# Performance work log

Hardware: AMD Instinct MI355X
Metric: run time of the kernel (lower is better)

The kernel has to match this reference:

```python
import jax, jax.numpy as jnp
import numpy as np

# Standard SMPL kinematic-tree parent indices (from kintree_table in the pkl)
PARENTS = np.array([-1, 0, 0, 0, 1, 2, 3, 4, 5, 6, 7, 8, 9, 9, 9, 12, 13, 14, 16, 17, 18, 19, 20, 21])
NJ = 24
NV = 6890  # SMPL template vertex count
N_POINTS = 2_000_000


def rodrigues(r):
    # r: (J,3) axis-angle -> (J,3,3) rotation matrices (eps matches torch's tiny noise regularizer)
    theta = jnp.linalg.norm(r, axis=1, keepdims=True) + 1e-8        # (J,1)
    rh = r / theta                                                   # (J,3)
    cos = jnp.cos(theta)[:, :, None]                                 # (J,1,1)
    sin = jnp.sin(theta)[:, :, None]
    z = jnp.zeros_like(rh[:, 0])
    K = jnp.stack([z, -rh[:, 2], rh[:, 1],
                   rh[:, 2], z, -rh[:, 0],
                   -rh[:, 1], rh[:, 0], z], axis=1).reshape(-1, 3, 3)
    outer = rh[:, :, None] * rh[:, None, :]
    return cos * jnp.eye(3, dtype=r.dtype) + (1.0 - cos) * outer + sin * K


def joint_transforms(beta, theta, shapedirs, v_template, J_regressor):
    # v_shaped: (6890,3); J: (24,3) joint locations
    v_shaped = jnp.einsum('vck,k->vc', shapedirs, beta) + v_template
    J = J_regressor @ v_shaped
    R = rodrigues(theta)                                             # (24,3,3)
    J_rel = jnp.concatenate([J[:1], J[1:] - J[PARENTS[1:]]], axis=0)
    bottom = jnp.broadcast_to(jnp.array([0., 0., 0., 1.], dtype=R.dtype), (NJ, 1, 4))
    local = jnp.concatenate([jnp.concatenate([R, J_rel[:, :, None]], axis=2), bottom], axis=1)  # (24,4,4)
    # chain along the fixed 24-joint kinematic tree
    res = [local[0]]
    for i in range(1, NJ):
        res.append(res[PARENTS[i]] @ local[i])
    G = jnp.stack(res, axis=0)                                       # (24,4,4)
    # subtract rest-pose joint translation (the 'pack' step)
    Jh = jnp.concatenate([J, jnp.zeros((NJ, 1), J.dtype)], axis=1)   # (24,4)
    t = jnp.einsum('jab,jb->ja', G, Jh)                              # (24,4)
    return G - jnp.concatenate([jnp.zeros((NJ, 4, 3), G.dtype), t[:, :, None]], axis=2)


def setup_inputs() -> dict:
    key = jax.random.key(0)
    ks = jax.random.split(key, 8)
    w = jax.random.uniform(ks[1], (NJ, N_POINTS), dtype=jnp.float32)
    w = w / jnp.sum(w, axis=0, keepdims=True)  # LBS weights sum to 1 per point
    return {
        'points': jax.random.normal(ks[0], (3, N_POINTS), dtype=jnp.float32),
        'weights': w,
        'beta': jax.random.normal(ks[2], (10,), dtype=jnp.float32),
        'theta': 0.3 * jax.random.normal(ks[3], (NJ, 3), dtype=jnp.float32),
        'da_theta': 0.3 * jax.random.normal(ks[4], (NJ, 3), dtype=jnp.float32),
        'shapedirs': 0.01 * jax.random.normal(ks[5], (NV, 3, 10), dtype=jnp.float32),
        'v_template': jax.random.normal(ks[6], (NV, 3), dtype=jnp.float32),
        'J_regressor': jax.random.uniform(ks[7], (NJ, NV), dtype=jnp.float32) / NV,
    }


def reference(points, weights, beta, theta, da_theta, shapedirs, v_template, J_regressor):
    # da_results: inverse rest ('da') pose transforms, built at init with beta = 0
    da = joint_transforms(jnp.zeros_like(beta), da_theta, shapedirs, v_template, J_regressor)
    da_inv = jnp.linalg.inv(da)                                      # (24,4,4)
    pose = joint_transforms(beta, theta, shapedirs, v_template, J_regressor)
    A = jnp.einsum('jab,jbc->jac', pose, da_inv)                     # (24,4,4)
    # weighted blend of joint transforms per point, then 4x4 matvec
    T = jnp.einsum('jn,jab->nab', weights, A)                        # (N,4,4)
    pts = points.T                                                   # (N,3)
    p_h = jnp.concatenate([pts, jnp.ones((pts.shape[0], 1), pts.dtype)], axis=1)  # (N,4)
    v = jnp.einsum('nab,nb->na', T, p_h)[:, :3]                      # (N,3)
    return v.T[None]                                                 # (1,3,N)
```

## Files before the change

kernel.cpp:

```cpp
#include <hip/hip_runtime.h>
#include <cmath>

#define NJ 24

__constant__ int PARENTS_c[NJ] = {-1, 0, 0, 0, 1, 2, 3, 4, 5, 6, 7, 8,
                                  9, 9, 9, 12, 13, 14, 16, 17, 18, 19, 20, 21};

__global__ __launch_bounds__(256) void joints_partial_kernel(
    const float* __restrict__ shapedirs,
    const float* __restrict__ v_template,
    const float* __restrict__ J_reg,
    const float* __restrict__ beta,
    float* __restrict__ Jpart, int NVv) {
  const int j = blockIdx.x;
  const int part = blockIdx.y;
  const int nparts = gridDim.y;

  __shared__ float sbeta[10];
  if (threadIdx.x < 10) sbeta[threadIdx.x] = beta[threadIdx.x];
  __syncthreads();

  const int v0 = (NVv * part) / nparts;
  const int v1 = (NVv * (part + 1)) / nparts;

  float acc[6] = {0.f, 0.f, 0.f, 0.f, 0.f, 0.f};
  for (int v = v0 + (int)threadIdx.x; v < v1; v += blockDim.x) {
    float w = J_reg[(size_t)j * NVv + v];
#pragma unroll
    for (int c = 0; c < 3; ++c) {
      float vtc = v_template[(size_t)v * 3 + c];
      float vs = vtc;
      const float* sd = shapedirs + ((size_t)v * 3 + c) * 10;
#pragma unroll
      for (int k = 0; k < 10; ++k) vs = fmaf(sd[k], sbeta[k], vs);
      acc[c] = fmaf(w, vs, acc[c]);
      acc[3 + c] = fmaf(w, vtc, acc[3 + c]);
    }
  }

#pragma unroll
  for (int c = 0; c < 6; ++c) {
    float x = acc[c];
#pragma unroll
    for (int off = 32; off > 0; off >>= 1) x += __shfl_down(x, off, 64);
    acc[c] = x;
  }
  __shared__ float wred[4][6];
  const int wave = threadIdx.x >> 6;
  const int lane = threadIdx.x & 63;
  if (lane == 0) {
#pragma unroll
    for (int c = 0; c < 6; ++c) wred[wave][c] = acc[c];
  }
  __syncthreads();
  if (threadIdx.x == 0) {
#pragma unroll
    for (int c = 0; c < 6; ++c) {
      float s = wred[0][c] + wred[1][c] + wred[2][c] + wred[3][c];
      Jpart[((size_t)j * nparts + part) * 6 + c] = s;
    }
  }
}

__device__ inline void rodrigues_local(double rx, double ry, double rz,
                                       double tx, double ty, double tz,
                                       double* L) {
  double th = sqrt(rx * rx + ry * ry + rz * rz) + 1e-8;
  double x = rx / th, y = ry / th, z = rz / th;
  double c = cos(th), s = sin(th), u = 1.0 - c;
  L[0] = c + u * x * x;  L[1] = u * x * y - s * z; L[2] = u * x * z + s * y; L[3] = tx;
  L[4] = u * x * y + s * z; L[5] = c + u * y * y;  L[6] = u * y * z - s * x; L[7] = ty;
  L[8] = u * x * z - s * y; L[9] = u * y * z + s * x; L[10] = c + u * z * z; L[11] = tz;
}

__device__ inline void affine_mul(const double* A, const double* B, double* C) {
#pragma unroll
  for (int r = 0; r < 3; ++r) {
#pragma unroll
    for (int cc = 0; cc < 3; ++cc)
      C[r * 4 + cc] = A[r * 4 + 0] * B[0 * 4 + cc] + A[r * 4 + 1] * B[1 * 4 + cc] +
                      A[r * 4 + 2] * B[2 * 4 + cc];
    C[r * 4 + 3] = A[r * 4 + 0] * B[3] + A[r * 4 + 1] * B[7] + A[r * 4 + 2] * B[11] +
                   A[r * 4 + 3];
  }
}

__device__ inline void inv3(const double* m, double* o) {
  double det = m[0] * (m[4] * m[8] - m[5] * m[7]) -
               m[1] * (m[3] * m[8] - m[5] * m[6]) +
               m[2] * (m[3] * m[7] - m[4] * m[6]);
  double id = 1.0 / det;
  o[0] = (m[4] * m[8] - m[5] * m[7]) * id;
  o[1] = (m[2] * m[7] - m[1] * m[8]) * id;
  o[2] = (m[1] * m[5] - m[2] * m[4]) * id;
  o[3] = (m[5] * m[6] - m[3] * m[8]) * id;
  o[4] = (m[0] * m[8] - m[2] * m[6]) * id;
  o[5] = (m[2] * m[3] - m[0] * m[5]) * id;
  o[6] = (m[3] * m[7] - m[4] * m[6]) * id;
  o[7] = (m[1] * m[6] - m[0] * m[7]) * id;
  o[8] = (m[0] * m[4] - m[1] * m[3]) * id;
}

__global__ __launch_bounds__(64) void transforms_kernel(
    const float* __restrict__ theta,
    const float* __restrict__ da_theta,
    const float* __restrict__ Jpart,
    int nparts,
    float* __restrict__ A_out) {
  __shared__ double J[NJ][3], J0[NJ][3];
  __shared__ double Lp[NJ][12], Ld[NJ][12], Gp[NJ][12], Gd[NJ][12];
  const int j = threadIdx.x;

  if (j < NJ) {
#pragma unroll
    for (int c = 0; c < 3; ++c) {
      double s = 0.0, s0 = 0.0;
      for (int p = 0; p < nparts; ++p) {
        s += (double)Jpart[(j * nparts + p) * 6 + c];
        s0 += (double)Jpart[(j * nparts + p) * 6 + 3 + c];
      }
      J[j][c] = s;
      J0[j][c] = s0;
    }
  }
  __syncthreads();

  if (j < NJ) {
    int par = PARENTS_c[j];
    double jx = J[j][0], jy = J[j][1], jz = J[j][2];
    double j0x = J0[j][0], j0y = J0[j][1], j0z = J0[j][2];
    if (par >= 0) {
      jx -= J[par][0]; jy -= J[par][1]; jz -= J[par][2];
      j0x -= J0[par][0]; j0y -= J0[par][1]; j0z -= J0[par][2];
    }
    rodrigues_local(theta[j * 3], theta[j * 3 + 1], theta[j * 3 + 2], jx, jy, jz, Lp[j]);
    rodrigues_local(da_theta[j * 3], da_theta[j * 3 + 1], da_theta[j * 3 + 2],
                    j0x, j0y, j0z, Ld[j]);
  }
  __syncthreads();

  if (threadIdx.x == 0) {
#pragma unroll
    for (int c = 0; c < 12; ++c) { Gp[0][c] = Lp[0][c]; Gd[0][c] = Ld[0][c]; }
    for (int i = 1; i < NJ; ++i) {
      int par = PARENTS_c[i];
      affine_mul(Gp[par], Lp[i], Gp[i]);
      affine_mul(Gd[par], Ld[i], Gd[i]);
    }
  }
  __syncthreads();

  if (j < NJ) {
    double P[12], D[12];
#pragma unroll
    for (int r = 0; r < 3; ++r) {
      double tp = Gp[j][r * 4 + 0] * J[j][0] + Gp[j][r * 4 + 1] * J[j][1] +
                  Gp[j][r * 4 + 2] * J[j][2];
      P[r * 4 + 0] = Gp[j][r * 4 + 0];
      P[r * 4 + 1] = Gp[j][r * 4 + 1];
      P[r * 4 + 2] = Gp[j][r * 4 + 2];
      P[r * 4 + 3] = Gp[j][r * 4 + 3] - tp;
      double td = Gd[j][r * 4 + 0] * J0[j][0] + Gd[j][r * 4 + 1] * J0[j][1] +
                  Gd[j][r * 4 + 2] * J0[j][2];
      D[r * 4 + 0] = Gd[j][r * 4 + 0];
      D[r * 4 + 1] = Gd[j][r * 4 + 1];
      D[r * 4 + 2] = Gd[j][r * 4 + 2];
      D[r * 4 + 3] = Gd[j][r * 4 + 3] - td;
    }
    double m[9] = {D[0], D[1], D[2], D[4], D[5], D[6], D[8], D[9], D[10]};
    double mi[9];
    inv3(m, mi);
    double it[3];
#pragma unroll
    for (int r = 0; r < 3; ++r)
      it[r] = -(mi[r * 3 + 0] * D[3] + mi[r * 3 + 1] * D[7] + mi[r * 3 + 2] * D[11]);
#pragma unroll
    for (int r = 0; r < 3; ++r) {
#pragma unroll
      for (int cc = 0; cc < 3; ++cc)
        A_out[j * 12 + r * 4 + cc] =
            (float)(P[r * 4 + 0] * mi[0 * 3 + cc] + P[r * 4 + 1] * mi[1 * 3 + cc] +
                    P[r * 4 + 2] * mi[2 * 3 + cc]);
      A_out[j * 12 + r * 4 + 3] =
          (float)(P[r * 4 + 0] * it[0] + P[r * 4 + 1] * it[1] +
                  P[r * 4 + 2] * it[2] + P[r * 4 + 3]);
    }
  }
}

__global__ __launch_bounds__(256) void lbs_kernel(
    const float* __restrict__ points,
    const float* __restrict__ weights,
    const float* __restrict__ A,
    float* __restrict__ out,
    int N) {
  __shared__ float sA[NJ * 12];
  for (int i = threadIdx.x; i < NJ * 12; i += blockDim.x) sA[i] = A[i];
  __syncthreads();

  const int tid = blockIdx.x * blockDim.x + threadIdx.x;
  const int n4 = tid * 4;
  if (n4 >= N) return;
  const size_t Ns = (size_t)N;

  if (n4 + 4 <= N) {
    float4 px = *(const float4*)(points + n4);
    float4 py = *(const float4*)(points + Ns + n4);
    float4 pz = *(const float4*)(points + 2 * Ns + n4);

    float4 T[12];
#pragma unroll
    for (int r = 0; r < 12; ++r) T[r] = make_float4(0.f, 0.f, 0.f, 0.f);

#pragma unroll
    for (int jj = 0; jj < NJ; ++jj) {
      float4 w = *(const float4*)(weights + (size_t)jj * Ns + n4);
#pragma unroll
      for (int r = 0; r < 12; ++r) {
        float a = sA[jj * 12 + r];
        T[r].x = fmaf(w.x, a, T[r].x);
        T[r].y = fmaf(w.y, a, T[r].y);
        T[r].z = fmaf(w.z, a, T[r].z);
        T[r].w = fmaf(w.w, a, T[r].w);
      }
    }

    float4 ox, oy, oz;
    ox.x = fmaf(T[0].x, px.x, fmaf(T[1].x, py.x, fmaf(T[2].x, pz.x, T[3].x)));
    ox.y = fmaf(T[0].y, px.y, fmaf(T[1].y, py.y, fmaf(T[2].y, pz.y, T[3].y)));
    ox.z = fmaf(T[0].z, px.z, fmaf(T[1].z, py.z, fmaf(T[2].z, pz.z, T[3].z)));
    ox.w = fmaf(T[0].w, px.w, fmaf(T[1].w, py.w, fmaf(T[2].w, pz.w, T[3].w)));
    oy.x = fmaf(T[4].x, px.x, fmaf(T[5].x, py.x, fmaf(T[6].x, pz.x, T[7].x)));
    oy.y = fmaf(T[4].y, px.y, fmaf(T[5].y, py.y, fmaf(T[6].y, pz.y, T[7].y)));
    oy.z = fmaf(T[4].z, px.z, fmaf(T[5].z, py.z, fmaf(T[6].z, pz.z, T[7].z)));
    oy.w = fmaf(T[4].w, px.w, fmaf(T[5].w, py.w, fmaf(T[6].w, pz.w, T[7].w)));
    oz.x = fmaf(T[8].x, px.x, fmaf(T[9].x, py.x, fmaf(T[10].x, pz.x, T[11].x)));
    oz.y = fmaf(T[8].y, px.y, fmaf(T[9].y, py.y, fmaf(T[10].y, pz.y, T[11].y)));
    oz.z = fmaf(T[8].z, px.z, fmaf(T[9].z, py.z, fmaf(T[10].z, pz.z, T[11].z)));
    oz.w = fmaf(T[8].w, px.w, fmaf(T[9].w, py.w, fmaf(T[10].w, pz.w, T[11].w)));

    *(float4*)(out + n4) = ox;
    *(float4*)(out + Ns + n4) = oy;
    *(float4*)(out + 2 * Ns + n4) = oz;
  } else {
    for (int n = n4; n < N; ++n) {
      float X = points[n], Y = points[Ns + n], Z = points[2 * Ns + n];
      float T[12];
#pragma unroll
      for (int r = 0; r < 12; ++r) T[r] = 0.f;
      for (int jj = 0; jj < NJ; ++jj) {
        float w = weights[(size_t)jj * Ns + n];
#pragma unroll
        for (int r = 0; r < 12; ++r) T[r] = fmaf(w, sA[jj * 12 + r], T[r]);
      }
      out[n] = fmaf(T[0], X, fmaf(T[1], Y, fmaf(T[2], Z, T[3])));
      out[Ns + n] = fmaf(T[4], X, fmaf(T[5], Y, fmaf(T[6], Z, T[7])));
      out[2 * Ns + n] = fmaf(T[8], X, fmaf(T[9], Y, fmaf(T[10], Z, T[11])));
    }
  }
}

extern "C" void kernel_launch(void* const* d_in, const int* in_sizes, int n_in,
                              void* d_out, int out_size, void* d_ws, size_t ws_size,
                              hipStream_t stream) {
  const float* points = (const float*)d_in[0];
  const float* weights = (const float*)d_in[1];
  const float* beta = (const float*)d_in[2];
  const float* theta = (const float*)d_in[3];
  const float* da_theta = (const float*)d_in[4];
  const float* shapedirs = (const float*)d_in[5];
  const float* v_template = (const float*)d_in[6];
  const float* J_regressor = (const float*)d_in[7];

  const int N = in_sizes[0] / 3;
  const int NVv = in_sizes[6] / 3;
  const int NPARTS = 8;

  float* ws = (float*)d_ws;
  float* A = ws;
  float* Jpart = ws + 512;

  dim3 gA(NJ, NPARTS);
  joints_partial_kernel<<<gA, 256, 0, stream>>>(shapedirs, v_template, J_regressor,
                                                beta, Jpart, NVv);
  transforms_kernel<<<1, 64, 0, stream>>>(theta, da_theta, Jpart, NPARTS, A);

  const int threads_total = (N + 3) / 4;
  const int blocks = (threads_total + 255) / 256;
  lbs_kernel<<<blocks, 256, 0, stream>>>(points, weights, A, (float*)d_out, N);
}
```

Baseline: 328.3 us.

## Parallelize kinematic chain per joint, use nontemporal LBS loads/stores, more J partitions

The serial single-thread kinematic chain is replaced by per-joint path walks over precomputed root-to-joint paths, with pose and rest chains handled by separate wavefronts of a 128-thread block. The LBS kernel switches to nontemporal vector loads and stores for points, weights and output so the streamed data bypasses cache retention. The joint-regression partition count doubles to spread that reduction over more blocks. The path walk repeats matrix products that the serial chain shared between joints, and the nontemporal hints may or may not help a purely streaming kernel.

Result: faster. 305.1 us (-7.1%).

```diff
diff --git a/kernel.cpp b/kernel.cpp
--- a/kernel.cpp
+++ b/kernel.cpp
@@ -3,8 +3,38 @@
 
 #define NJ 24
 
+typedef float f4 __attribute__((ext_vector_type(4)));
+
 __constant__ int PARENTS_c[NJ] = {-1, 0, 0, 0, 1, 2, 3, 4, 5, 6, 7, 8,
                                   9, 9, 9, 12, 13, 14, 16, 17, 18, 19, 20, 21};
+
+__constant__ signed char PATHS_c[NJ][9] = {
+    {0, 0, 0, 0, 0, 0, 0, 0, 0},
+    {0, 1, 0, 0, 0, 0, 0, 0, 0},
+    {0, 2, 0, 0, 0, 0, 0, 0, 0},
+    {0, 3, 0, 0, 0, 0, 0, 0, 0},
+    {0, 1, 4, 0, 0, 0, 0, 0, 0},
+    {0, 2, 5, 0, 0, 0, 0, 0, 0},
+    {0, 3, 6, 0, 0, 0, 0, 0, 0},
+    {0, 1, 4, 7, 0, 0, 0, 0, 0},
+    {0, 2, 5, 8, 0, 0, 0, 0, 0},
+    {0, 3, 6, 9, 0, 0, 0, 0, 0},
+    {0, 1, 4, 7, 10, 0, 0, 0, 0},
+    {0, 2, 5, 8, 11, 0, 0, 0, 0},
+    {0, 3, 6, 9, 12, 0, 0, 0, 0},
+    {0, 3, 6, 9, 13, 0, 0, 0, 0},
+    {0, 3, 6, 9, 14, 0, 0, 0, 0},
+    {0, 3, 6, 9, 12, 15, 0, 0, 0},
+    {0, 3, 6, 9, 13, 16, 0, 0, 0},
+    {0, 3, 6, 9, 14, 17, 0, 0, 0},
+    {0, 3, 6, 9, 13, 16, 18, 0, 0},
+    {0, 3, 6, 9, 14, 17, 19, 0, 0},
+    {0, 3, 6, 9, 13, 16, 18, 20, 0},
+    {0, 3, 6, 9, 14, 17, 19, 21, 0},
+    {0, 3, 6, 9, 13, 16, 18, 20, 22},
+    {0, 3, 6, 9, 14, 17, 19, 21, 23}};
+__constant__ signed char PLEN_c[NJ] = {1, 2, 2, 2, 3, 3, 3, 4, 4, 4, 5, 5,
+                                       5, 5, 5, 6, 6, 6, 7, 7, 8, 8, 9, 9};
 
 __global__ __launch_bounds__(256) void joints_partial_kernel(
     const float* __restrict__ shapedirs,
@@ -82,6 +112,19 @@
                       A[r * 4 + 2] * B[2 * 4 + cc];
     C[r * 4 + 3] = A[r * 4 + 0] * B[3] + A[r * 4 + 1] * B[7] + A[r * 4 + 2] * B[11] +
                    A[r * 4 + 3];
+  }
+}
+
+__device__ inline void chain_walk(const double (*L)[12], int jj, double* M) {
+  const signed char* path = PATHS_c[jj];
+  const int len = PLEN_c[jj];
+#pragma unroll
+  for (int c = 0; c < 12; ++c) M[c] = L[path[0]][c];
+  for (int k = 1; k < len; ++k) {
+    double T[12];
+    affine_mul(M, L[path[k]], T);
+#pragma unroll
+    for (int c = 0; c < 12; ++c) M[c] = T[c];
   }
 }
 
@@ -101,7 +144,7 @@
   o[8] = (m[0] * m[4] - m[1] * m[3]) * id;
 }
 
-__global__ __launch_bounds__(64) void transforms_kernel(
+__global__ __launch_bounds__(128) void transforms_kernel(
     const float* __restrict__ theta,
     const float* __restrict__ da_theta,
     const float* __restrict__ Jpart,
@@ -109,48 +152,54 @@
     float* __restrict__ A_out) {
   __shared__ double J[NJ][3], J0[NJ][3];
   __shared__ double Lp[NJ][12], Ld[NJ][12], Gp[NJ][12], Gd[NJ][12];
-  const int j = threadIdx.x;
-
-  if (j < NJ) {
+  const int t = threadIdx.x;
+
+  if (t < NJ) {
 #pragma unroll
     for (int c = 0; c < 3; ++c) {
       double s = 0.0, s0 = 0.0;
       for (int p = 0; p < nparts; ++p) {
-        s += (double)Jpart[(j * nparts + p) * 6 + c];
-        s0 += (double)Jpart[(j * nparts + p) * 6 + 3 + c];
+        s += (double)Jpart[(t * nparts + p) * 6 + c];
+        s0 += (double)Jpart[(t * nparts + p) * 6 + 3 + c];
       }
-      J[j][c] = s;
-      J0[j][c] = s0;
-    }
-  }
-  __syncthreads();
-
-  if (j < NJ) {
+      J[t][c] = s;
+      J0[t][c] = s0;
+    }
+  }
+  __syncthreads();
+
+  if (t < NJ) {
+    const int j = t;
     int par = PARENTS_c[j];
     double jx = J[j][0], jy = J[j][1], jz = J[j][2];
+    if (par >= 0) { jx -= J[par][0]; jy -= J[par][1]; jz -= J[par][2]; }
+    rodrigues_local(theta[j * 3], theta[j * 3 + 1], theta[j * 3 + 2], jx, jy, jz, Lp[j]);
+  } else if (t >= 64 && t < 64 + NJ) {
+    const int j = t - 64;
+    int par = PARENTS_c[j];
     double j0x = J0[j][0], j0y = J0[j][1], j0z = J0[j][2];
-    if (par >= 0) {
-      jx -= J[par][0]; jy -= J[par][1]; jz -= J[par][2];
-      j0x -= J0[par][0]; j0y -= J0[par][1]; j0z -= J0[par][2];
-    }
-    rodrigues_local(theta[j * 3], theta[j * 3 + 1], theta[j * 3 + 2], jx, jy, jz, Lp[j]);
+    if (par >= 0) { j0x -= J0[par][0]; j0y -= J0[par][1]; j0z -= J0[par][2]; }
     rodrigues_local(da_theta[j * 3], da_theta[j * 3 + 1], da_theta[j * 3 + 2],
                     j0x, j0y, j0z, Ld[j]);
   }
   __syncthreads();
 
-  if (threadIdx.x == 0) {
-#pragma unroll
-    for (int c = 0; c < 12; ++c) { Gp[0][c] = Lp[0][c]; Gd[0][c] = Ld[0][c]; }
-    for (int i = 1; i < NJ; ++i) {
-      int par = PARENTS_c[i];
-      affine_mul(Gp[par], Lp[i], Gp[i]);
-      affine_mul(Gd[par], Ld[i], Gd[i]);
-    }
-  }
-  __syncthreads();
-
-  if (j < NJ) {
+  if (t < NJ) {
+    double M[12];
+    chain_walk(Lp, t, M);
+#pragma unroll
+    for (int c = 0; c < 12; ++c) Gp[t][c] = M[c];
+  } else if (t >= 64 && t < 64 + NJ) {
+    const int j = t - 64;
+    double M[12];
+    chain_walk(Ld, j, M);
+#pragma unroll
+    for (int c = 0; c < 12; ++c) Gd[j][c] = M[c];
+  }
+  __syncthreads();
+
+  if (t < NJ) {
+    const int j = t;
     double P[12], D[12];
 #pragma unroll
     for (int r = 0; r < 3; ++r) {
@@ -204,17 +253,17 @@
   const size_t Ns = (size_t)N;
 
   if (n4 + 4 <= N) {
-    float4 px = *(const float4*)(points + n4);
-    float4 py = *(const float4*)(points + Ns + n4);
-    float4 pz = *(const float4*)(points + 2 * Ns + n4);
-
-    float4 T[12];
-#pragma unroll
-    for (int r = 0; r < 12; ++r) T[r] = make_float4(0.f, 0.f, 0.f, 0.f);
+    f4 px = __builtin_nontemporal_load((const f4*)(points + n4));
+    f4 py = __builtin_nontemporal_load((const f4*)(points + Ns + n4));
+    f4 pz = __builtin_nontemporal_load((const f4*)(points + 2 * Ns + n4));
+
+    f4 T[12];
+#pragma unroll
+    for (int r = 0; r < 12; ++r) T[r] = (f4)(0.f);
 
 #pragma unroll
     for (int jj = 0; jj < NJ; ++jj) {
-      float4 w = *(const float4*)(weights + (size_t)jj * Ns + n4);
+      f4 w = __builtin_nontemporal_load((const f4*)(weights + (size_t)jj * Ns + n4));
 #pragma unroll
       for (int r = 0; r < 12; ++r) {
         float a = sA[jj * 12 + r];
@@ -225,23 +274,23 @@
       }
     }
 
-    float4 ox, oy, oz;
+    f4 ox, oy, oz;
     ox.x = fmaf(T[0].x, px.x, fmaf(T[1].x, py.x, fmaf(T[2].x, pz.x, T[3].x)));
     ox.y = fmaf(T[0].y, px.y, fmaf(T[1].y, py.y, fmaf(T[2].y, pz.y, T[3].y)));
     ox.z = fmaf(T[0].z, px.z, fmaf(T[1].z, py.z, fmaf(T[2].z, pz.z, T[3].z)));
     ox.w = fmaf(T[0].w, px.w, fmaf(T[1].w, py.w, fmaf(T[2].w, pz.w, T[3].w)));
     oy.x = fmaf(T[4].x, px.x, fmaf(T[5].x, py.x, fmaf(T[6].x, pz.x, T[7].x)));
     oy.y = fmaf(T[4].y, px.y, fmaf(T[5].y, py.y, fmaf(T[6].y, pz.y, T[7].y)));
-    oy.z = fmaf(T[4].z, px.z, fmaf(T[5].z, py.z, fmaf(T[6].z, pz.z, T[7].z)));
+    oy.z = fmaf(T[4].z, px.z, fmaf(T[6 - 1].z, py.z, fmaf(T[6].z, pz.z, T[7].z)));
     oy.w = fmaf(T[4].w, px.w, fmaf(T[5].w, py.w, fmaf(T[6].w, pz.w, T[7].w)));
     oz.x = fmaf(T[8].x, px.x, fmaf(T[9].x, py.x, fmaf(T[10].x, pz.x, T[11].x)));
     oz.y = fmaf(T[8].y, px.y, fmaf(T[9].y, py.y, fmaf(T[10].y, pz.y, T[11].y)));
     oz.z = fmaf(T[8].z, px.z, fmaf(T[9].z, py.z, fmaf(T[10].z, pz.z, T[11].z)));
     oz.w = fmaf(T[8].w, px.w, fmaf(T[9].w, py.w, fmaf(T[10].w, pz.w, T[11].w)));
 
-    *(float4*)(out + n4) = ox;
-    *(float4*)(out + Ns + n4) = oy;
-    *(float4*)(out + 2 * Ns + n4) = oz;
+    __builtin_nontemporal_store(ox, (f4*)(out + n4));
+    __builtin_nontemporal_store(oy, (f4*)(out + Ns + n4));
+    __builtin_nontemporal_store(oz, (f4*)(out + 2 * Ns + n4));
   } else {
     for (int n = n4; n < N; ++n) {
       float X = points[n], Y = points[Ns + n], Z = points[2 * Ns + n];
@@ -274,7 +323,7 @@
 
   const int N = in_sizes[0] / 3;
   const int NVv = in_sizes[6] / 3;
-  const int NPARTS = 8;
+  const int NPARTS = 16;
 
   float* ws = (float*)d_ws;
   float* A = ws;
@@ -283,7 +332,7 @@
   dim3 gA(NJ, NPARTS);
   joints_partial_kernel<<<gA, 256, 0, stream>>>(shapedirs, v_template, J_regressor,
                                                 beta, Jpart, NVv);
-  transforms_kernel<<<1, 64, 0, stream>>>(theta, da_theta, Jpart, NPARTS, A);
+  transforms_kernel<<<1, 128, 0, stream>>>(theta, da_theta, Jpart, NPARTS, A);
 
   const int threads_total = (N + 3) / 4;
   const int blocks = (threads_total + 255) / 256;
```
